# Kernel optimization log

Hardware: AMD Instinct MI355X
Metric: run time of the kernel (lower is better)

The kernel has to match this reference:

```python
import jax, jax.numpy as jnp
import numpy as np
import math

B, C, H, W, D = 4, 128, 32, 32, 32
HEADS = 4
N = H * W * D            # input_size = 32768
NG = 64                  # global token count, fixed by EF1 shape (64, skip_proj)
SKIP_PROJ = C // HEADS   # 32, required by output reshape
PROJ = C // HEADS        # 32, required by attn @ v_proj contraction
LN_EPS = 1e-5


def setup_inputs() -> dict:
    key = jax.random.key(0)
    k0, k1, k2, k3, k4 = jax.random.split(key, 5)
    std1 = 1.0 / math.sqrt(SKIP_PROJ)
    std2 = 1.0 / math.sqrt(PROJ)
    return {
        "skip": jax.random.normal(k0, (B, C, H, W, D), jnp.float32),
        "out": jax.random.normal(k1, (B, C, H, W, D), jnp.float32),
        "global_fea": jax.random.normal(k2, (B, NG, C), jnp.float32),
        "ln_w": jnp.ones((C,), jnp.float32),
        "ln_b": jnp.zeros((C,), jnp.float32),
        "temperature3": jnp.ones((HEADS, 1, 1), jnp.float32),
        "EF1": jax.random.uniform(k3, (NG, SKIP_PROJ), jnp.float32, -std1, std1),
        "EF2": jax.random.uniform(k4, (N, PROJ), jnp.float32, -std2, std2),
    }


def _layernorm(x, w, b):
    mu = jnp.mean(x, axis=-1, keepdims=True)
    var = jnp.var(x, axis=-1, keepdims=True)
    return (x - mu) * jax.lax.rsqrt(var + LN_EPS) * w + b


def reference(skip, out, global_fea, ln_w, ln_b, temperature3, EF1, EF2):
    b, c, h_, w_, d_ = skip.shape
    n = h_ * w_ * d_
    nh = temperature3.shape[0]
    dh = c // nh
    # (B,C,H,W,D) -> (B,N,C)
    skip_t = skip.reshape(b, c, n).transpose(0, 2, 1)
    out_t = out.reshape(b, c, n).transpose(0, 2, 1)
    skip_n = _layernorm(skip_t, ln_w, ln_b)
    out_n = _layernorm(out_t, ln_w, ln_b)
    # heads: (B,N,C) -> (B,h,d,N)
    q = out_n.reshape(b, n, nh, dh).transpose(0, 2, 3, 1)
    k = skip_n.reshape(b, n, nh, dh).transpose(0, 2, 3, 1)
    v = global_fea.reshape(b, -1, nh, dh).transpose(0, 2, 3, 1)  # (B,h,d,NG)
    v_proj = jnp.einsum('bhdn,nk->bhdk', v, EF1)   # (B,h,d,SKIP_PROJ)
    k_proj = jnp.einsum('bhdn,nk->bhdk', k, EF2)   # (B,h,d,PROJ)
    # q^T k_proj: (B,h,N,PROJ), scaled by per-head temperature
    attn = jnp.einsum('bhdn,bhdp->bhnp', q, k_proj) * temperature3
    attn = jax.nn.softmax(attn, axis=-1)
    # attn @ v_proj contracts PROJ with the d axis of v_proj (PROJ == d)
    x = jnp.einsum('bhnp,bhpk->bhnk', attn, v_proj)   # (B,h,N,SKIP_PROJ)
    x = x.transpose(0, 3, 1, 2).reshape(b, n, c)       # (B,N,C)
    # (B,N,C) -> (B,C,H,W,D)
    return x.reshape(b, h_, w_, d_, c).transpose(0, 4, 1, 2, 3)
```

## Files before the change

kernel.cpp:

```cpp
#include <hip/hip_runtime.h>
#include <hip/hip_bf16.h>

#define NN 32768
#define LN_EPS 1e-5f

typedef float v4f __attribute__((ext_vector_type(4)));
typedef __attribute__((ext_vector_type(8))) short bf16x8;
typedef __attribute__((ext_vector_type(4))) float f32x4;

__device__ __forceinline__ void bsplit(float f, short &hi, short &lo) {
  unsigned u; __builtin_memcpy(&u, &f, 4);
  unsigned hb = u & 0xffff0000u;
  hi = (short)(u >> 16);
  float hf; __builtin_memcpy(&hf, &hb, 4);
  float lf = f - hf;
  unsigned ul; __builtin_memcpy(&ul, &lf, 4);
  lo = (short)(ul >> 16);
}

__device__ __forceinline__ unsigned short bf16u(float f) {
  unsigned u; __builtin_memcpy(&u, &f, 4);
  return (unsigned short)(u >> 16);
}

__global__ __launch_bounds__(256) void k1_mfma(
    const float* __restrict__ skip, const float* __restrict__ EF2,
    float* __restrict__ partials)
{
  __shared__ float cred[4752];

  int bx = blockIdx.x, t = threadIdx.x;
  int b = bx >> 7, chunk = bx & 127;
  int w = t >> 6, l = t & 63;
  int i16 = l & 15, kc = (l >> 4) << 3;

  f32x4 acc[9][2];
#pragma unroll
  for (int mt = 0; mt < 9; ++mt)
#pragma unroll
    for (int nt = 0; nt < 2; ++nt)
      acc[mt][nt] = (f32x4){0.f, 0.f, 0.f, 0.f};

#pragma unroll
  for (int it = 0; it < 2; ++it) {
    int n0 = chunk * 256 + w * 64 + it * 32;
    int kt = chunk * 8 + w * 2 + it;

    bf16x8 Bh[2], Bl[2];
    const float* eb = EF2 + (size_t)(kt * 32 + kc) * 32;
#pragma unroll
    for (int nt = 0; nt < 2; ++nt) {
#pragma unroll
      for (int j = 0; j < 8; ++j) {
        float e = eb[(size_t)j * 32 + nt * 16 + i16];
        short hh, ll; bsplit(e, hh, ll);
        Bh[nt][j] = hh; Bl[nt][j] = ll;
      }
    }

    const float* ap = skip + (size_t)(b * 128) * NN + n0 + kc;
    float af[8][8];
#pragma unroll
    for (int mt = 0; mt < 8; ++mt) {
      const float* rp = ap + (size_t)(mt * 16 + i16) * NN;
      float4 a0 = *(const float4*)(rp);
      float4 a1 = *(const float4*)(rp + 4);
      af[mt][0] = a0.x; af[mt][1] = a0.y; af[mt][2] = a0.z; af[mt][3] = a0.w;
      af[mt][4] = a1.x; af[mt][5] = a1.y; af[mt][6] = a1.z; af[mt][7] = a1.w;
    }

    float cs[8], sq[8];
#pragma unroll
    for (int j = 0; j < 8; ++j) {
      float s = 0.f, q = 0.f;
#pragma unroll
      for (int mt = 0; mt < 8; ++mt) { s += af[mt][j]; q = fmaf(af[mt][j], af[mt][j], q); }
      cs[j] = s; sq[j] = q;
    }
#pragma unroll
    for (int m = 1; m <= 8; m <<= 1) {
#pragma unroll
      for (int j = 0; j < 8; ++j) {
        cs[j] += __shfl_xor(cs[j], m);
        sq[j] += __shfl_xor(sq[j], m);
      }
    }
    float rs[8], mr[8];
#pragma unroll
    for (int j = 0; j < 8; ++j) {
      float mu = cs[j] * (1.f / 128.f);
      rs[j] = rsqrtf(sq[j] * (1.f / 128.f) - mu * mu + LN_EPS);
      mr[j] = mu * rs[j];
    }

#pragma unroll
    for (int mt = 0; mt < 8; ++mt) {
      bf16x8 Ah, Al;
#pragma unroll
      for (int j = 0; j < 8; ++j) {
        short h, lo; bsplit(af[mt][j] * rs[j], h, lo);
        Ah[j] = h; Al[j] = lo;
      }
#pragma unroll
      for (int nt = 0; nt < 2; ++nt) {
        acc[mt][nt] = __builtin_amdgcn_mfma_f32_16x16x32_bf16(Ah, Bh[nt], acc[mt][nt], 0, 0, 0);
        acc[mt][nt] = __builtin_amdgcn_mfma_f32_16x16x32_bf16(Al, Bh[nt], acc[mt][nt], 0, 0, 0);
        acc[mt][nt] = __builtin_amdgcn_mfma_f32_16x16x32_bf16(Ah, Bl[nt], acc[mt][nt], 0, 0, 0);
      }
    }
    {
      bf16x8 Ah, Al;
#pragma unroll
      for (int j = 0; j < 8; ++j) {
        float v = (i16 == 0) ? mr[j] : ((i16 == 1) ? 1.f : 0.f);
        short h, lo; bsplit(v, h, lo);
        Ah[j] = h; Al[j] = lo;
      }
#pragma unroll
      for (int nt = 0; nt < 2; ++nt) {
        acc[8][nt] = __builtin_amdgcn_mfma_f32_16x16x32_bf16(Ah, Bh[nt], acc[8][nt], 0, 0, 0);
        acc[8][nt] = __builtin_amdgcn_mfma_f32_16x16x32_bf16(Al, Bh[nt], acc[8][nt], 0, 0, 0);
        acc[8][nt] = __builtin_amdgcn_mfma_f32_16x16x32_bf16(Ah, Bl[nt], acc[8][nt], 0, 0, 0);
      }
    }
  }

  int rbase = (l >> 4) * 4;
  for (int ww = 0; ww < 4; ++ww) {
    __syncthreads();
    if (w == ww) {
#pragma unroll
      for (int mt = 0; mt < 9; ++mt)
#pragma unroll
        for (int nt = 0; nt < 2; ++nt)
#pragma unroll
          for (int r = 0; r < 4; ++r) {
            int addr = (mt * 16 + rbase + r) * 33 + nt * 16 + i16;
            if (ww == 0) cred[addr] = acc[mt][nt][r];
            else         cred[addr] += acc[mt][nt][r];
          }
    }
  }
  __syncthreads();
  float* pw = partials + (size_t)bx * 4608;
#pragma unroll
  for (int i = 0; i < 18; ++i) {
    int idx = t + i * 256;
    pw[idx] = cred[(idx >> 5) * 33 + (idx & 31)];
  }
}

__global__ __launch_bounds__(256) void k2_red(
    const float* __restrict__ partials, float* __restrict__ raw)
{
  __shared__ float red[8][32];
  int row = blockIdx.x;
  int b   = blockIdx.y;
  int t = threadIdx.x;
  int p = t & 31, grp = t >> 5;
  const float* pp = partials + ((size_t)(b * 128 + grp * 16)) * 4608 + row * 32 + p;
  float s = 0.f;
  for (int i = 0; i < 16; ++i)
    s += pp[(size_t)i * 4608];
  red[grp][p] = s;
  __syncthreads();
  if (t < 32) {
    float tot = 0.f;
#pragma unroll
    for (int g2 = 0; g2 < 8; ++g2) tot += red[g2][t];
    raw[((size_t)b * 130 + row) * 32 + t] = tot;
  }
}

__global__ __launch_bounds__(64) void k2_post(
    const float* __restrict__ raw, const float* __restrict__ gf,
    const float* __restrict__ EF1, const float* __restrict__ lnw,
    const float* __restrict__ lnb,
    float* __restrict__ W1, float* __restrict__ B1,
    short* __restrict__ kfrag, short* __restrict__ vfrag)
{
  __shared__ float kpw_s[32][33];
  __shared__ float vps_s[32][33];
  int bh = blockIdx.x, l = threadIdx.x;
  int b = bh >> 2, h = bh & 3;
  int p = l & 31, half = l >> 5;
  const float* rb = raw + (size_t)b * 130 * 32;
  float T = rb[128 * 32 + p];
  float U = rb[129 * 32 + p];
  float w1a = 0.f, b1a = 0.f;
#pragma unroll
  for (int d2 = 0; d2 < 16; ++d2) {
    int d = half * 16 + d2, c = h * 32 + d;
    float tot = rb[c * 32 + p];
    float kp = lnw[c] * (tot - T) + lnb[c] * U;
    float kw = lnw[c] * kp;
    kpw_s[d][p] = kw;
    w1a += kw;
    b1a += lnb[c] * kp;
  }
  w1a += __shfl_xor(w1a, 32);
  b1a += __shfl_xor(b1a, 32);
  if (half == 0) {
    W1[bh * 32 + p] = w1a;
    B1[bh * 32 + p] = b1a;
  }
  {
    float acc[16];
#pragma unroll
    for (int kk = 0; kk < 16; ++kk) acc[kk] = 0.f;
    for (int g = 0; g < 64; ++g) {
      float gv = gf[((size_t)(b * 64 + g)) * 128 + h * 32 + p];
      const float* e1 = EF1 + g * 32 + half * 16;
#pragma unroll
      for (int kk = 0; kk < 16; ++kk) acc[kk] += gv * e1[kk];
    }
#pragma unroll
    for (int kk = 0; kk < 16; ++kk) vps_s[p][half * 16 + kk] = acc[kk];
  }
  __syncthreads();
  int i16 = l & 15, g4 = l >> 4;
#pragma unroll
  for (int pt = 0; pt < 2; ++pt) {
    bf16x8 hi8, lo8;
#pragma unroll
    for (int j = 0; j < 8; ++j) {
      short hh, ll; bsplit(kpw_s[g4 * 8 + j][pt * 16 + i16], hh, ll);
      hi8[j] = hh; lo8[j] = ll;
    }
    *(bf16x8*)(kfrag + (size_t)bh * 2048 + pt * 1024 + l * 8) = hi8;
    *(bf16x8*)(kfrag + (size_t)bh * 2048 + pt * 1024 + 512 + l * 8) = lo8;
  }
#pragma unroll
  for (int kt = 0; kt < 2; ++kt) {
    bf16x8 hi8, lo8;
#pragma unroll
    for (int j = 0; j < 8; ++j) {
      short hh, ll; bsplit(vps_s[g4 * 8 + j][kt * 16 + i16], hh, ll);
      hi8[j] = hh; lo8[j] = ll;
    }
    *(bf16x8*)(vfrag + (size_t)bh * 2048 + kt * 1024 + l * 8) = hi8;
    *(bf16x8*)(vfrag + (size_t)bh * 2048 + kt * 1024 + 512 + l * 8) = lo8;
  }
}

__global__ __launch_bounds__(256) void k3_attn(
    const float* __restrict__ outp, const short* __restrict__ kfrag,
    const short* __restrict__ vfrag, const float* __restrict__ W1,
    const float* __restrict__ B1, const float* __restrict__ temp,
    __hip_bfloat16* __restrict__ xws)
{
  __shared__ float q_lds[32 * 132];
  __shared__ float2 sst[32];
  __shared__ float sstp[4][2][32];
  __shared__ unsigned p32[4][272];

  int bx = blockIdx.x, t = threadIdx.x;
  int w = t >> 6, l = t & 63;
  int b = bx >> 10, chunk = bx & 1023;
  int n0 = chunk * 32;
  int i16 = l & 15, g4 = l >> 4;
  int nq = (t & 7) * 4, cb = t >> 3;

  const float* qb = outp + (size_t)b * 128 * NN + n0;
  float s4[4] = {0.f, 0.f, 0.f, 0.f}, q24[4] = {0.f, 0.f, 0.f, 0.f};
#pragma unroll
  for (int pass = 0; pass < 4; ++pass) {
    int c = pass * 32 + cb;
    float4 v = *(const float4*)(qb + (size_t)c * NN + nq);
    q_lds[(nq + 0) * 132 + c] = v.x;
    q_lds[(nq + 1) * 132 + c] = v.y;
    q_lds[(nq + 2) * 132 + c] = v.z;
    q_lds[(nq + 3) * 132 + c] = v.w;
    s4[0] += v.x; q24[0] = fmaf(v.x, v.x, q24[0]);
    s4[1] += v.y; q24[1] = fmaf(v.y, v.y, q24[1]);
    s4[2] += v.z; q24[2] = fmaf(v.z, v.z, q24[2]);
    s4[3] += v.w; q24[3] = fmaf(v.w, v.w, q24[3]);
  }
#pragma unroll
  for (int m = 8; m <= 32; m <<= 1) {
#pragma unroll
    for (int k = 0; k < 4; ++k) {
      s4[k] += __shfl_xor(s4[k], m);
      q24[k] += __shfl_xor(q24[k], m);
    }
  }
  if ((l & 56) == 0) {
    *(float4*)&sstp[w][0][nq] = (float4){s4[0], s4[1], s4[2], s4[3]};
    *(float4*)&sstp[w][1][nq] = (float4){q24[0], q24[1], q24[2], q24[3]};
  }
  __syncthreads();
  if (t < 32) {
    float s  = sstp[0][0][t] + sstp[1][0][t] + sstp[2][0][t] + sstp[3][0][t];
    float q2 = sstp[0][1][t] + sstp[1][1][t] + sstp[2][1][t] + sstp[3][1][t];
    float mu = s * (1.f / 128.f);
    float rsv = rsqrtf(q2 * (1.f / 128.f) - mu * mu + LN_EPS);
    sst[t] = make_float2(mu, rsv);
  }
  __syncthreads();

  int h = w;
  const short* kfb = kfrag + (size_t)((b * 4 + h) * 2048);
  const short* vfb = vfrag + (size_t)((b * 4 + h) * 2048);
  bf16x8 KAh[2], KAl[2], VAh[2], VAl[2];
#pragma unroll
  for (int pt = 0; pt < 2; ++pt) {
    KAh[pt] = *(const bf16x8*)(kfb + pt * 1024 + l * 8);
    KAl[pt] = *(const bf16x8*)(kfb + pt * 1024 + 512 + l * 8);
    VAh[pt] = *(const bf16x8*)(vfb + pt * 1024 + l * 8);
    VAl[pt] = *(const bf16x8*)(vfb + pt * 1024 + 512 + l * 8);
  }
  float w1v[8], b1v[8];
#pragma unroll
  for (int pt = 0; pt < 2; ++pt)
#pragma unroll
    for (int r = 0; r < 4; ++r) {
      int p = g4 * 4 + r + pt * 16;
      w1v[pt * 4 + r] = W1[(b * 4 + h) * 32 + p];
      b1v[pt * 4 + r] = B1[(b * 4 + h) * 32 + p];
    }
  float tm = temp[h];
  unsigned* pwv = &p32[w][0];
  f32x4 Xs[2][2];

#pragma unroll
  for (int nt2 = 0; nt2 < 2; ++nt2) {
    int nrow = nt2 * 16 + i16;
    float2 mr = sst[nrow];

    const float* qrow = &q_lds[nrow * 132 + h * 32 + g4 * 8];
    float4 qa = *(const float4*)(qrow);
    float4 qb4 = *(const float4*)(qrow + 4);
    float qf[8] = {qa.x, qa.y, qa.z, qa.w, qb4.x, qb4.y, qb4.z, qb4.w};
    bf16x8 QBh, QBl;
#pragma unroll
    for (int jj = 0; jj < 8; ++jj) {
      short hh, ll; bsplit(qf[jj], hh, ll);
      QBh[jj] = hh; QBl[jj] = ll;
    }

    f32x4 C[2];
#pragma unroll
    for (int pt = 0; pt < 2; ++pt) {
      C[pt] = (f32x4){0.f, 0.f, 0.f, 0.f};
      C[pt] = __builtin_amdgcn_mfma_f32_16x16x32_bf16(KAh[pt], QBh, C[pt], 0, 0, 0);
      C[pt] = __builtin_amdgcn_mfma_f32_16x16x32_bf16(KAl[pt], QBh, C[pt], 0, 0, 0);
      C[pt] = __builtin_amdgcn_mfma_f32_16x16x32_bf16(KAh[pt], QBl, C[pt], 0, 0, 0);
    }

    float lg[8];
#pragma unroll
    for (int pt = 0; pt < 2; ++pt)
#pragma unroll
      for (int r = 0; r < 4; ++r)
        lg[pt * 4 + r] = tm * (mr.y * C[pt][r] - mr.y * mr.x * w1v[pt * 4 + r] + b1v[pt * 4 + r]);
    float mx = lg[0];
#pragma unroll
    for (int i = 1; i < 8; ++i) mx = fmaxf(mx, lg[i]);
    mx = fmaxf(mx, __shfl_xor(mx, 16));
    mx = fmaxf(mx, __shfl_xor(mx, 32));
    float sum = 0.f;
#pragma unroll
    for (int i = 0; i < 8; ++i) { float e = __expf(lg[i] - mx); lg[i] = e; sum += e; }
    sum += __shfl_xor(sum, 16);
    sum += __shfl_xor(sum, 32);
    float inv = 1.f / sum;
#pragma unroll
    for (int i = 0; i < 8; ++i) lg[i] *= inv;

#pragma unroll
    for (int pt = 0; pt < 2; ++pt)
#pragma unroll
      for (int pr = 0; pr < 2; ++pr) {
        unsigned wlo = bf16u(lg[pt * 4 + pr * 2]);
        unsigned whi = bf16u(lg[pt * 4 + pr * 2 + 1]);
        pwv[(pt * 8 + g4 * 2 + pr) * 17 + i16] = (whi << 16) | wlo;
      }
    __builtin_amdgcn_wave_barrier();
    bf16x8 PBh;
#pragma unroll
    for (int jw = 0; jw < 4; ++jw) {
      unsigned wv = pwv[(g4 * 4 + jw) * 17 + i16];
      PBh[2 * jw]     = (short)(wv & 0xffffu);
      PBh[2 * jw + 1] = (short)(wv >> 16);
    }
    __builtin_amdgcn_wave_barrier();

#pragma unroll
    for (int kt = 0; kt < 2; ++kt) {
      f32x4 X = (f32x4){0.f, 0.f, 0.f, 0.f};
      X = __builtin_amdgcn_mfma_f32_16x16x32_bf16(VAh[kt], PBh, X, 0, 0, 0);
      X = __builtin_amdgcn_mfma_f32_16x16x32_bf16(VAl[kt], PBh, X, 0, 0, 0);
      Xs[nt2][kt] = X;
    }
  }

  short* xwb = (short*)xws + (((size_t)((b * 4 + h) * 32)) << 15) + n0 + i16 * 2;
#pragma unroll
  for (int kt = 0; kt < 2; ++kt)
#pragma unroll
    for (int r = 0; r < 4; ++r) {
      int k = kt * 16 + g4 * 4 + r;
      unsigned pkd = ((unsigned)bf16u(Xs[1][kt][r]) << 16) | (unsigned)bf16u(Xs[0][kt][r]);
      *(unsigned*)(xwb + ((size_t)k << 15)) = pkd;
    }
}

__global__ __launch_bounds__(256) void k4_scatter(
    const __hip_bfloat16* __restrict__ xws, float* __restrict__ outd)
{
  __shared__ float tile[64][129];
  int bx = blockIdx.x;
  int tg = bx & 3;
  int k = (bx >> 2) & 31;
  int h = (bx >> 7) & 3;
  int b = bx >> 9;
  int t = threadIdx.x;
  const unsigned* src32 = (const unsigned*)((const short*)xws +
      (((size_t)((b * 4 + h) * 32 + k)) << 15) + tg * 8192);
  for (int i2 = t; i2 < 4096; i2 += 256) {
    unsigned v = src32[i2];
    int loc = ((i2 >> 4) << 5) | (i2 & 15);
    unsigned lo = v & 0xffffu, hi = v >> 16;
    __hip_bfloat16 blo, bhi;
    __builtin_memcpy(&blo, &lo, 2);
    __builtin_memcpy(&bhi, &hi, 2);
    tile[loc >> 7][loc & 127] = __bfloat162float(blo);
    int loc2 = loc + 16;
    tile[loc2 >> 7][loc2 & 127] = __bfloat162float(bhi);
  }
  __syncthreads();
  int nh = t & 63, cq = t >> 6;
  size_t obase = (size_t)b * 128 * NN + (size_t)k * 1024 + h * 256 + tg * 64 + nh;
  for (int i = 0; i < 32; ++i) {
    int c0 = i * 4 + cq;
    outd[obase + (size_t)c0 * NN] = tile[nh][c0];
  }
}

extern "C" void kernel_launch(void* const* d_in, const int* in_sizes, int n_in,
                              void* d_out, int out_size, void* d_ws, size_t ws_size,
                              hipStream_t stream) {
  const float* skip = (const float*)d_in[0];
  const float* outp = (const float*)d_in[1];
  const float* gf   = (const float*)d_in[2];
  const float* lnw  = (const float*)d_in[3];
  const float* lnb  = (const float*)d_in[4];
  const float* temp = (const float*)d_in[5];
  const float* EF1  = (const float*)d_in[6];
  const float* EF2  = (const float*)d_in[7];
  float* outd = (float*)d_out;
  char* ws = (char*)d_ws;

  __hip_bfloat16* xws = (__hip_bfloat16*)ws;
  float* partials = (float*)ws;
  float* raw   = outd + 524288;
  float* W1    = outd + 540928;
  float* B1    = outd + 541440;
  short* kfrag = (short*)(outd + 541952);
  short* vfrag = (short*)(outd + 558336);

  k1_mfma<<<512, 256, 0, stream>>>(skip, EF2, partials);
  k2_red<<<dim3(130, 4), 256, 0, stream>>>(partials, raw);
  k2_post<<<16, 64, 0, stream>>>(raw, gf, EF1, lnw, lnb, W1, B1, kfrag, vfrag);
  k3_attn<<<4096, 256, 0, stream>>>(outp, kfrag, vfrag, W1, B1, temp, xws);
  k4_scatter<<<2048, 256, 0, stream>>>(xws, outd);
}
```

Before: 73.43 us.

## Load q tile directly into LDS via global_load_lds with XOR swizzle

Replaces the register-staged transposed store of the query tile into padded shared memory with direct global-to-LDS loads into a linear, XOR-swizzled layout. LayerNorm statistics are then computed from LDS afterwards, and each thread finishes its own per-row reduction instead of a single-warp finalize pass with an extra barrier. The K/V fragment loads are issued before the barrier so they overlap the asynchronous LDS fill. The aim is to cut VGPR traffic and bank-conflicted scattered LDS writes. In exchange, the 8 q values per thread are now read with scalar LDS loads instead of float4 loads, and the mean/rstd arithmetic is repeated in every thread.

```diff
diff --git a/kernel.cpp b/kernel.cpp
--- a/kernel.cpp
+++ b/kernel.cpp
@@ -249,9 +249,8 @@
     const float* __restrict__ B1, const float* __restrict__ temp,
     __hip_bfloat16* __restrict__ xws)
 {
-  __shared__ float q_lds[32 * 132];
-  __shared__ float2 sst[32];
-  __shared__ float sstp[4][2][32];
+  __shared__ float q_lin[4096];
+  __shared__ float sstp[2][32][4];
   __shared__ unsigned p32[4][272];
 
   int bx = blockIdx.x, t = threadIdx.x;
@@ -259,44 +258,21 @@
   int b = bx >> 10, chunk = bx & 1023;
   int n0 = chunk * 32;
   int i16 = l & 15, g4 = l >> 4;
-  int nq = (t & 7) * 4, cb = t >> 3;
-
-  const float* qb = outp + (size_t)b * 128 * NN + n0;
-  float s4[4] = {0.f, 0.f, 0.f, 0.f}, q24[4] = {0.f, 0.f, 0.f, 0.f};
-#pragma unroll
-  for (int pass = 0; pass < 4; ++pass) {
-    int c = pass * 32 + cb;
-    float4 v = *(const float4*)(qb + (size_t)c * NN + nq);
-    q_lds[(nq + 0) * 132 + c] = v.x;
-    q_lds[(nq + 1) * 132 + c] = v.y;
-    q_lds[(nq + 2) * 132 + c] = v.z;
-    q_lds[(nq + 3) * 132 + c] = v.w;
-    s4[0] += v.x; q24[0] = fmaf(v.x, v.x, q24[0]);
-    s4[1] += v.y; q24[1] = fmaf(v.y, v.y, q24[1]);
-    s4[2] += v.z; q24[2] = fmaf(v.z, v.z, q24[2]);
-    s4[3] += v.w; q24[3] = fmaf(v.w, v.w, q24[3]);
-  }
-#pragma unroll
-  for (int m = 8; m <= 32; m <<= 1) {
-#pragma unroll
-    for (int k = 0; k < 4; ++k) {
-      s4[k] += __shfl_xor(s4[k], m);
-      q24[k] += __shfl_xor(q24[k], m);
-    }
-  }
-  if ((l & 56) == 0) {
-    *(float4*)&sstp[w][0][nq] = (float4){s4[0], s4[1], s4[2], s4[3]};
-    *(float4*)&sstp[w][1][nq] = (float4){q24[0], q24[1], q24[2], q24[3]};
-  }
-  __syncthreads();
-  if (t < 32) {
-    float s  = sstp[0][0][t] + sstp[1][0][t] + sstp[2][0][t] + sstp[3][0][t];
-    float q2 = sstp[0][1][t] + sstp[1][1][t] + sstp[2][1][t] + sstp[3][1][t];
-    float mu = s * (1.f / 128.f);
-    float rsv = rsqrtf(q2 * (1.f / 128.f) - mu * mu + LN_EPS);
-    sst[t] = make_float2(mu, rsv);
-  }
-  __syncthreads();
+
+  {
+    const float* gb = outp + (size_t)b * 128 * NN + n0;
+    int r = l >> 3, nb = l & 7;
+#pragma unroll
+    for (int i = 0; i < 4; ++i) {
+      int c = w * 32 + i * 8 + r;
+      int g = nb ^ ((c >> 2) & 7);
+      const float* src = gb + (size_t)c * NN + g * 4;
+      __builtin_amdgcn_global_load_lds(
+          (const __attribute__((address_space(1))) void*)src,
+          (__attribute__((address_space(3))) void*)&q_lin[(w * 32 + i * 8) * 32],
+          16, 0, 0);
+    }
+  }
 
   int h = w;
   const short* kfb = kfrag + (size_t)((b * 4 + h) * 2048);
@@ -322,15 +298,54 @@
   unsigned* pwv = &p32[w][0];
   f32x4 Xs[2][2];
 
+  __syncthreads();
+
+  {
+    int ng = l & 7, ch = l >> 3;
+    float s4[4] = {0.f, 0.f, 0.f, 0.f}, q24[4] = {0.f, 0.f, 0.f, 0.f};
+#pragma unroll
+    for (int ci = 0; ci < 4; ++ci) {
+      int c = ch * 16 + w * 4 + ci;
+      f32x4 v = *(const f32x4*)&q_lin[c * 32 + ((ng ^ ((c >> 2) & 7)) * 4)];
+#pragma unroll
+      for (int m = 0; m < 4; ++m) { s4[m] += v[m]; q24[m] = fmaf(v[m], v[m], q24[m]); }
+    }
+#pragma unroll
+    for (int m = 8; m <= 32; m <<= 1) {
+#pragma unroll
+      for (int k2 = 0; k2 < 4; ++k2) {
+        s4[k2] += __shfl_xor(s4[k2], m);
+        q24[k2] += __shfl_xor(q24[k2], m);
+      }
+    }
+    if (ch == 0) {
+#pragma unroll
+      for (int m = 0; m < 4; ++m) {
+        sstp[0][ng * 4 + m][w] = s4[m];
+        sstp[1][ng * 4 + m][w] = q24[m];
+      }
+    }
+  }
+  __syncthreads();
+
 #pragma unroll
   for (int nt2 = 0; nt2 < 2; ++nt2) {
-    int nrow = nt2 * 16 + i16;
-    float2 mr = sst[nrow];
-
-    const float* qrow = &q_lds[nrow * 132 + h * 32 + g4 * 8];
-    float4 qa = *(const float4*)(qrow);
-    float4 qb4 = *(const float4*)(qrow + 4);
-    float qf[8] = {qa.x, qa.y, qa.z, qa.w, qb4.x, qb4.y, qb4.z, qb4.w};
+    int nloc = nt2 * 16 + i16;
+    float4 sv = *(const float4*)&sstp[0][nloc][0];
+    float4 qv = *(const float4*)&sstp[1][nloc][0];
+    float s  = (sv.x + sv.y) + (sv.z + sv.w);
+    float q2 = (qv.x + qv.y) + (qv.z + qv.w);
+    float mu = s * (1.f / 128.f);
+    float rsv = rsqrtf(q2 * (1.f / 128.f) - mu * mu + LN_EPS);
+
+    int nbh = nt2 * 4 + (i16 >> 2);
+    int nlo = i16 & 3;
+    float qf[8];
+#pragma unroll
+    for (int jj = 0; jj < 8; ++jj) {
+      int c = h * 32 + g4 * 8 + jj;
+      qf[jj] = q_lin[c * 32 + ((nbh ^ ((c >> 2) & 7)) * 4) + nlo];
+    }
     bf16x8 QBh, QBl;
 #pragma unroll
     for (int jj = 0; jj < 8; ++jj) {
@@ -352,7 +367,7 @@
     for (int pt = 0; pt < 2; ++pt)
 #pragma unroll
       for (int r = 0; r < 4; ++r)
-        lg[pt * 4 + r] = tm * (mr.y * C[pt][r] - mr.y * mr.x * w1v[pt * 4 + r] + b1v[pt * 4 + r]);
+        lg[pt * 4 + r] = tm * (rsv * C[pt][r] - rsv * mu * w1v[pt * 4 + r] + b1v[pt * 4 + r]);
     float mx = lg[0];
 #pragma unroll
     for (int i = 1; i < 8; ++i) mx = fmaxf(mx, lg[i]);
```

Result: no change. 73.98 us (+0.7%).

## Enlarge attention tile to 128 tokens per 512-thread block with linear LDS staging

Applied to the files above, without the earlier changes.

The attention kernel now handles 128 tokens per block with 8 waves instead of 32 tokens with 4 waves. The query tile is stored in LDS in channel-major order with full float4 stores rather than a scattered transpose. Each wave processes two 32-token sub-chunks for its head, so K/V fragments and per-head constants are reused across more tokens and fewer blocks are launched. In exchange, LDS use per block rises to about 75 KB, which may limit occupancy, and reading 8 channels per token is now a strided scalar LDS gather.

```diff
diff --git a/kernel.cpp b/kernel.cpp
--- a/kernel.cpp
+++ b/kernel.cpp
@@ -243,62 +243,49 @@
   }
 }
 
-__global__ __launch_bounds__(256) void k3_attn(
+__global__ __launch_bounds__(512) void k3_attn(
     const float* __restrict__ outp, const short* __restrict__ kfrag,
     const short* __restrict__ vfrag, const float* __restrict__ W1,
     const float* __restrict__ B1, const float* __restrict__ temp,
     __hip_bfloat16* __restrict__ xws)
 {
-  __shared__ float q_lds[32 * 132];
-  __shared__ float2 sst[32];
-  __shared__ float sstp[4][2][32];
-  __shared__ unsigned p32[4][272];
+  __shared__ float q_lin[128 * 129];
+  __shared__ float scratch[2304];
 
   int bx = blockIdx.x, t = threadIdx.x;
   int w = t >> 6, l = t & 63;
-  int b = bx >> 10, chunk = bx & 1023;
-  int n0 = chunk * 32;
+  int b = bx >> 8, chunk = bx & 255;
+  int n0 = chunk * 128;
   int i16 = l & 15, g4 = l >> 4;
-  int nq = (t & 7) * 4, cb = t >> 3;
-
-  const float* qb = outp + (size_t)b * 128 * NN + n0;
+  int lj = l & 31, halfw = l >> 5;
+
+  const float* gb = outp + (size_t)b * 128 * NN + n0;
   float s4[4] = {0.f, 0.f, 0.f, 0.f}, q24[4] = {0.f, 0.f, 0.f, 0.f};
-#pragma unroll
-  for (int pass = 0; pass < 4; ++pass) {
-    int c = pass * 32 + cb;
-    float4 v = *(const float4*)(qb + (size_t)c * NN + nq);
-    q_lds[(nq + 0) * 132 + c] = v.x;
-    q_lds[(nq + 1) * 132 + c] = v.y;
-    q_lds[(nq + 2) * 132 + c] = v.z;
-    q_lds[(nq + 3) * 132 + c] = v.w;
+  int hw = 2 * w + halfw;
+#pragma unroll
+  for (int p = 0; p < 8; ++p) {
+    int c = p * 16 + hw;
+    float4 v = *(const float4*)(gb + (size_t)c * NN + lj * 4);
+    *(float4*)&q_lin[c * 129 + lj * 4] = v;
     s4[0] += v.x; q24[0] = fmaf(v.x, v.x, q24[0]);
     s4[1] += v.y; q24[1] = fmaf(v.y, v.y, q24[1]);
     s4[2] += v.z; q24[2] = fmaf(v.z, v.z, q24[2]);
     s4[3] += v.w; q24[3] = fmaf(v.w, v.w, q24[3]);
   }
 #pragma unroll
-  for (int m = 8; m <= 32; m <<= 1) {
-#pragma unroll
-    for (int k = 0; k < 4; ++k) {
-      s4[k] += __shfl_xor(s4[k], m);
-      q24[k] += __shfl_xor(q24[k], m);
-    }
-  }
-  if ((l & 56) == 0) {
-    *(float4*)&sstp[w][0][nq] = (float4){s4[0], s4[1], s4[2], s4[3]};
-    *(float4*)&sstp[w][1][nq] = (float4){q24[0], q24[1], q24[2], q24[3]};
-  }
-  __syncthreads();
-  if (t < 32) {
-    float s  = sstp[0][0][t] + sstp[1][0][t] + sstp[2][0][t] + sstp[3][0][t];
-    float q2 = sstp[0][1][t] + sstp[1][1][t] + sstp[2][1][t] + sstp[3][1][t];
-    float mu = s * (1.f / 128.f);
-    float rsv = rsqrtf(q2 * (1.f / 128.f) - mu * mu + LN_EPS);
-    sst[t] = make_float2(mu, rsv);
-  }
-  __syncthreads();
-
-  int h = w;
+  for (int k2 = 0; k2 < 4; ++k2) {
+    s4[k2] += __shfl_xor(s4[k2], 32);
+    q24[k2] += __shfl_xor(q24[k2], 32);
+  }
+  if (halfw == 0) {
+#pragma unroll
+    for (int k2 = 0; k2 < 4; ++k2) {
+      scratch[(4 * lj + k2) * 9 + w] = s4[k2];
+      scratch[1152 + (4 * lj + k2) * 9 + w] = q24[k2];
+    }
+  }
+
+  int h = w & 3, sqb = w >> 2;
   const short* kfb = kfrag + (size_t)((b * 4 + h) * 2048);
   const short* vfb = vfrag + (size_t)((b * 4 + h) * 2048);
   bf16x8 KAh[2], KAl[2], VAh[2], VAl[2];
@@ -319,90 +306,114 @@
       b1v[pt * 4 + r] = B1[(b * 4 + h) * 32 + p];
     }
   float tm = temp[h];
-  unsigned* pwv = &p32[w][0];
-  f32x4 Xs[2][2];
-
-#pragma unroll
-  for (int nt2 = 0; nt2 < 2; ++nt2) {
-    int nrow = nt2 * 16 + i16;
-    float2 mr = sst[nrow];
-
-    const float* qrow = &q_lds[nrow * 132 + h * 32 + g4 * 8];
-    float4 qa = *(const float4*)(qrow);
-    float4 qb4 = *(const float4*)(qrow + 4);
-    float qf[8] = {qa.x, qa.y, qa.z, qa.w, qb4.x, qb4.y, qb4.z, qb4.w};
-    bf16x8 QBh, QBl;
-#pragma unroll
-    for (int jj = 0; jj < 8; ++jj) {
-      short hh, ll; bsplit(qf[jj], hh, ll);
-      QBh[jj] = hh; QBl[jj] = ll;
-    }
-
-    f32x4 C[2];
-#pragma unroll
-    for (int pt = 0; pt < 2; ++pt) {
-      C[pt] = (f32x4){0.f, 0.f, 0.f, 0.f};
-      C[pt] = __builtin_amdgcn_mfma_f32_16x16x32_bf16(KAh[pt], QBh, C[pt], 0, 0, 0);
-      C[pt] = __builtin_amdgcn_mfma_f32_16x16x32_bf16(KAl[pt], QBh, C[pt], 0, 0, 0);
-      C[pt] = __builtin_amdgcn_mfma_f32_16x16x32_bf16(KAh[pt], QBl, C[pt], 0, 0, 0);
-    }
-
-    float lg[8];
-#pragma unroll
-    for (int pt = 0; pt < 2; ++pt)
-#pragma unroll
-      for (int r = 0; r < 4; ++r)
-        lg[pt * 4 + r] = tm * (mr.y * C[pt][r] - mr.y * mr.x * w1v[pt * 4 + r] + b1v[pt * 4 + r]);
-    float mx = lg[0];
-#pragma unroll
-    for (int i = 1; i < 8; ++i) mx = fmaxf(mx, lg[i]);
-    mx = fmaxf(mx, __shfl_xor(mx, 16));
-    mx = fmaxf(mx, __shfl_xor(mx, 32));
-    float sum = 0.f;
-#pragma unroll
-    for (int i = 0; i < 8; ++i) { float e = __expf(lg[i] - mx); lg[i] = e; sum += e; }
-    sum += __shfl_xor(sum, 16);
-    sum += __shfl_xor(sum, 32);
-    float inv = 1.f / sum;
-#pragma unroll
-    for (int i = 0; i < 8; ++i) lg[i] *= inv;
-
-#pragma unroll
-    for (int pt = 0; pt < 2; ++pt)
-#pragma unroll
-      for (int pr = 0; pr < 2; ++pr) {
-        unsigned wlo = bf16u(lg[pt * 4 + pr * 2]);
-        unsigned whi = bf16u(lg[pt * 4 + pr * 2 + 1]);
-        pwv[(pt * 8 + g4 * 2 + pr) * 17 + i16] = (whi << 16) | wlo;
-      }
-    __builtin_amdgcn_wave_barrier();
-    bf16x8 PBh;
-#pragma unroll
-    for (int jw = 0; jw < 4; ++jw) {
-      unsigned wv = pwv[(g4 * 4 + jw) * 17 + i16];
-      PBh[2 * jw]     = (short)(wv & 0xffffu);
-      PBh[2 * jw + 1] = (short)(wv >> 16);
-    }
-    __builtin_amdgcn_wave_barrier();
-
-#pragma unroll
-    for (int kt = 0; kt < 2; ++kt) {
-      f32x4 X = (f32x4){0.f, 0.f, 0.f, 0.f};
-      X = __builtin_amdgcn_mfma_f32_16x16x32_bf16(VAh[kt], PBh, X, 0, 0, 0);
-      X = __builtin_amdgcn_mfma_f32_16x16x32_bf16(VAl[kt], PBh, X, 0, 0, 0);
-      Xs[nt2][kt] = X;
-    }
-  }
-
-  short* xwb = (short*)xws + (((size_t)((b * 4 + h) * 32)) << 15) + n0 + i16 * 2;
-#pragma unroll
-  for (int kt = 0; kt < 2; ++kt)
-#pragma unroll
-    for (int r = 0; r < 4; ++r) {
-      int k = kt * 16 + g4 * 4 + r;
-      unsigned pkd = ((unsigned)bf16u(Xs[1][kt][r]) << 16) | (unsigned)bf16u(Xs[0][kt][r]);
-      *(unsigned*)(xwb + ((size_t)k << 15)) = pkd;
-    }
+
+  __syncthreads();
+
+  float2 mrr[4];
+#pragma unroll
+  for (int uu = 0; uu < 4; ++uu) {
+    int sc2 = sqb + (uu >> 1) * 2;
+    int nl = sc2 * 32 + (uu & 1) * 16 + i16;
+    float s = 0.f, q2 = 0.f;
+#pragma unroll
+    for (int j = 0; j < 8; ++j) {
+      s  += scratch[nl * 9 + j];
+      q2 += scratch[1152 + nl * 9 + j];
+    }
+    float mu = s * (1.f / 128.f);
+    mrr[uu] = make_float2(mu, rsqrtf(q2 * (1.f / 128.f) - mu * mu + LN_EPS));
+  }
+  __syncthreads();
+
+  unsigned* pwv = (unsigned*)scratch + w * 272;
+
+#pragma unroll
+  for (int unit = 0; unit < 2; ++unit) {
+    int sc2 = sqb + unit * 2;
+    f32x4 Xs[2][2];
+#pragma unroll
+    for (int nt2 = 0; nt2 < 2; ++nt2) {
+      float2 mr = mrr[unit * 2 + nt2];
+      int nloc = sc2 * 32 + nt2 * 16 + i16;
+
+      float qf[8];
+#pragma unroll
+      for (int jj = 0; jj < 8; ++jj)
+        qf[jj] = q_lin[(h * 32 + g4 * 8 + jj) * 129 + nloc];
+      bf16x8 QBh, QBl;
+#pragma unroll
+      for (int jj = 0; jj < 8; ++jj) {
+        short hh, ll; bsplit(qf[jj], hh, ll);
+        QBh[jj] = hh; QBl[jj] = ll;
+      }
+
+      f32x4 C[2];
+#pragma unroll
+      for (int pt = 0; pt < 2; ++pt) {
+        C[pt] = (f32x4){0.f, 0.f, 0.f, 0.f};
+        C[pt] = __builtin_amdgcn_mfma_f32_16x16x32_bf16(KAh[pt], QBh, C[pt], 0, 0, 0);
+        C[pt] = __builtin_amdgcn_mfma_f32_16x16x32_bf16(KAl[pt], QBh, C[pt], 0, 0, 0);
+        C[pt] = __builtin_amdgcn_mfma_f32_16x16x32_bf16(KAh[pt], QBl, C[pt], 0, 0, 0);
+      }
+
+      float lg[8];
+#pragma unroll
+      for (int pt = 0; pt < 2; ++pt)
+#pragma unroll
+        for (int r = 0; r < 4; ++r)
+          lg[pt * 4 + r] = tm * (mr.y * C[pt][r] - mr.y * mr.x * w1v[pt * 4 + r] + b1v[pt * 4 + r]);
+      float mx = lg[0];
+#pragma unroll
+      for (int i = 1; i < 8; ++i) mx = fmaxf(mx, lg[i]);
+      mx = fmaxf(mx, __shfl_xor(mx, 16));
+      mx = fmaxf(mx, __shfl_xor(mx, 32));
+      float sum = 0.f;
+#pragma unroll
+      for (int i = 0; i < 8; ++i) { float e = __expf(lg[i] - mx); lg[i] = e; sum += e; }
+      sum += __shfl_xor(sum, 16);
+      sum += __shfl_xor(sum, 32);
+      float inv = 1.f / sum;
+#pragma unroll
+      for (int i = 0; i < 8; ++i) lg[i] *= inv;
+
+#pragma unroll
+      for (int pt = 0; pt < 2; ++pt)
+#pragma unroll
+        for (int pr = 0; pr < 2; ++pr) {
+          unsigned wlo = bf16u(lg[pt * 4 + pr * 2]);
+          unsigned whi = bf16u(lg[pt * 4 + pr * 2 + 1]);
+          pwv[(pt * 8 + g4 * 2 + pr) * 17 + i16] = (whi << 16) | wlo;
+        }
+      __builtin_amdgcn_wave_barrier();
+      bf16x8 PBh;
+#pragma unroll
+      for (int jw = 0; jw < 4; ++jw) {
+        unsigned wv = pwv[(g4 * 4 + jw) * 17 + i16];
+        PBh[2 * jw]     = (short)(wv & 0xffffu);
+        PBh[2 * jw + 1] = (short)(wv >> 16);
+      }
+      __builtin_amdgcn_wave_barrier();
+
+#pragma unroll
+      for (int kt = 0; kt < 2; ++kt) {
+        f32x4 X = (f32x4){0.f, 0.f, 0.f, 0.f};
+        X = __builtin_amdgcn_mfma_f32_16x16x32_bf16(VAh[kt], PBh, X, 0, 0, 0);
+        X = __builtin_amdgcn_mfma_f32_16x16x32_bf16(VAl[kt], PBh, X, 0, 0, 0);
+        Xs[nt2][kt] = X;
+      }
+    }
+
+    short* xwb = (short*)xws + (((size_t)((b * 4 + h) * 32)) << 15)
+               + n0 + sc2 * 32 + i16 * 2;
+#pragma unroll
+    for (int kt = 0; kt < 2; ++kt)
+#pragma unroll
+      for (int r = 0; r < 4; ++r) {
+        int k = kt * 16 + g4 * 4 + r;
+        unsigned pkd = ((unsigned)bf16u(Xs[1][kt][r]) << 16) | (unsigned)bf16u(Xs[0][kt][r]);
+        *(unsigned*)(xwb + ((size_t)k << 15)) = pkd;
+      }
+  }
 }
 
 __global__ __launch_bounds__(256) void k4_scatter(
@@ -462,6 +473,6 @@
   k1_mfma<<<512, 256, 0, stream>>>(skip, EF2, partials);
   k2_red<<<dim3(130, 4), 256, 0, stream>>>(partials, raw);
   k2_post<<<16, 64, 0, stream>>>(raw, gf, EF1, lnw, lnb, W1, B1, kfrag, vfrag);
-  k3_attn<<<4096, 256, 0, stream>>>(outp, kfrag, vfrag, W1, B1, temp, xws);
+  k3_attn<<<1024, 512, 0, stream>>>(outp, kfrag, vfrag, W1, B1, temp, xws);
   k4_scatter<<<2048, 256, 0, stream>>>(xws, outd);
 }
```

New measurement: 76.43 us. 1.04x slower.
